# Kernel optimization log

Hardware: AMD Instinct MI355X
Metric: run time of the kernel (lower is better)

Reference implementation:

```python
import jax, jax.numpy as jnp
import numpy as np

EPS = 1e-12  # matches torch F.normalize clamp_min eps


def agnn_conv(x, src, dst, beta, num_nodes):
    # x: [N, H]; src/dst: [E'] (self-loops already included)
    norm = jnp.sqrt(jnp.sum(x * x, axis=-1, keepdims=True))
    x_norm = x / jnp.maximum(norm, EPS)
    # edge-wise cosine similarity scaled by beta
    logits = beta * jnp.sum(x_norm[src] * x_norm[dst], axis=-1)  # [E']
    # scatter-softmax over incoming edges of each destination node
    m = jax.ops.segment_max(logits, dst, num_segments=num_nodes)  # [N]
    e = jnp.exp(logits - m[dst])
    s = jax.ops.segment_sum(e, dst, num_segments=num_nodes)       # [N]
    alpha = e / s[dst]                                            # [E']
    # weighted scatter-add aggregation of source features
    return jax.ops.segment_sum(alpha[:, None] * x[src], dst, num_segments=num_nodes)


def setup_inputs() -> dict:
    key = jax.random.key(0)
    ks = jax.random.split(key, 8)
    N, E, C_in, C_hid, C_out = 100000, 1600000, 512, 128, 64
    x = jax.random.normal(ks[0], (N, C_in), dtype=jnp.float32)
    edge_index = jax.random.randint(ks[1], (2, E), 0, N, dtype=jnp.int64)
    W1 = jax.random.normal(ks[2], (C_in, C_hid), dtype=jnp.float32) / np.sqrt(C_in)
    b1 = jnp.zeros((C_hid,), dtype=jnp.float32)
    W2 = jax.random.normal(ks[3], (C_hid, C_out), dtype=jnp.float32) / np.sqrt(C_hid)
    b2 = jnp.zeros((C_out,), dtype=jnp.float32)
    beta2 = jnp.array(1.0, dtype=jnp.float32)  # learned beta of prop2; prop1 beta fixed at 1.0
    return {"x": x, "edge_index": edge_index, "W1": W1, "b1": b1,
            "beta2": beta2, "W2": W2, "b2": b2}


def reference(x, edge_index, W1, b1, beta2, W2, b2):
    N = x.shape[0]
    # AGNNConv adds self-loops by default
    loops = jnp.arange(N, dtype=edge_index.dtype)
    src = jnp.concatenate([edge_index[0], loops])
    dst = jnp.concatenate([edge_index[1], loops])
    # dropout is identity in eval mode
    h = jax.nn.relu(x @ W1 + b1)                      # [N, hidden]
    h = agnn_conv(h, src, dst, jnp.float32(1.0), N)   # prop1 (beta frozen = 1)
    h = agnn_conv(h, src, dst, beta2, N)              # prop2 (learned beta)
    logits = h @ W2 + b2                              # [N, out]
    return jax.nn.log_softmax(logits, axis=1)
```

## Files before the change

### kernel.cpp

```cpp
#include <hip/hip_runtime.h>
#include <hip/hip_fp8.h>
#include <math.h>


static inline int divup(int a, int b) { return (a + b - 1) / b; }

typedef __attribute__((ext_vector_type(8))) short short8;
typedef __attribute__((ext_vector_type(4))) float f32x4;
union U16 { uint4 u; short8 s; };

__device__ __forceinline__ unsigned bf16r(float f) {
    unsigned u = __float_as_uint(f);
    return (u + 0x7FFFu + ((u >> 16) & 1u)) >> 16;
}
__device__ __forceinline__ unsigned pack2(float a, float b) {
    return bf16r(a) | (bf16r(b) << 16);
}
__device__ __forceinline__ float bflo(unsigned u) { return __uint_as_float(u << 16); }
__device__ __forceinline__ float bfhi(unsigned u) { return __uint_as_float(u & 0xFFFF0000u); }

__device__ __forceinline__ unsigned char fp8e(float f) {
    __hip_fp8_e4m3 q(f);
    return (unsigned char)q.__x;
}
__device__ __forceinline__ float fp8d(unsigned char b) {
    __hip_fp8_e4m3 q;
    q.__x = (__hip_fp8_storage_t)b;
    return (float)q;
}
__device__ __forceinline__ void unpf8(uint2 u, float* v) {
    const unsigned char* b = (const unsigned char*)&u;
#pragma unroll
    for (int i = 0; i < 8; ++i) v[i] = fp8d(b[i]);
}

__global__ __launch_bounds__(64) void k_detect(const int* __restrict__ raw, int* flag) {
    int t = threadIdx.x;
    int v = raw[2 * t + 1];
    unsigned long long b = __ballot(v != 0);
    if (t == 0) *flag = (b == 0ULL) ? 1 : 0;
}

__global__ __launch_bounds__(256) void k_cvt(const int* __restrict__ raw, int E,
                                             const int* __restrict__ flag,
                                             int* __restrict__ s32, int* __restrict__ d32,
                                             int* __restrict__ cnt) {
    int i = blockIdx.x * blockDim.x + threadIdx.x;
    if (i >= E) return;
    int s, d;
    if (*flag) {
        s = raw[2 * (size_t)i];
        d = raw[2 * ((size_t)E + i)];
    } else {
        s = raw[i];
        d = raw[(size_t)E + i];
    }
    s32[i] = s;
    d32[i] = d;
    atomicAdd(&cnt[d], 1);
}

__global__ __launch_bounds__(1024) void k_scan1(const int* __restrict__ cnt, int N,
                                                int* __restrict__ rp, int* __restrict__ bsum) {
    __shared__ int sm[1024];
    int t = threadIdx.x;
    int i = blockIdx.x * 1024 + t;
    int v = (i < N) ? cnt[i] + 1 : 0;
    sm[t] = v;
    __syncthreads();
#pragma unroll
    for (int off = 1; off < 1024; off <<= 1) {
        int u = (t >= off) ? sm[t - off] : 0;
        __syncthreads();
        sm[t] += u;
        __syncthreads();
    }
    if (i < N) rp[i] = sm[t] - v;
    if (t == 1023) bsum[blockIdx.x] = sm[t];
}

__global__ __launch_bounds__(64) void k_scan2(int* __restrict__ bsum, int nb) {
    if (threadIdx.x == 0) {
        int run = 0;
        for (int i = 0; i < nb; ++i) { int v = bsum[i]; bsum[i] = run; run += v; }
    }
}

__global__ __launch_bounds__(256) void k_scan3(int* __restrict__ rp, const int* __restrict__ bsum,
                                               int N, int Etot, int* __restrict__ cursor) {
    int i = blockIdx.x * blockDim.x + threadIdx.x;
    if (i < N) {
        int v = rp[i] + bsum[i >> 10];
        rp[i] = v;
        cursor[i] = v;
    } else if (i == N) {
        rp[N] = Etot;
    }
}

__global__ __launch_bounds__(256) void k_scatter(const int* __restrict__ s32,
                                                 const int* __restrict__ d32, int E, int N,
                                                 int* __restrict__ cursor,
                                                 int* __restrict__ esrc) {
    int b = blockIdx.x;
    int xcd = b & 7;
    int nstripe = gridDim.x >> 3;
    int stripe = b >> 3;
    int lo = (int)(((long long)xcd * N) >> 3);
    int hi = (int)(((long long)(xcd + 1) * N) >> 3);
    int Etot = E + N;
    for (int e = stripe * 256 + threadIdx.x; e < Etot; e += nstripe * 256) {
        int d = (e < E) ? d32[e] : (e - E);
        if (d < lo || d >= hi) continue;
        int s = (e < E) ? s32[e] : d;
        int pos = atomicAdd(&cursor[d], 1);
        esrc[pos] = s;
    }
}

__global__ __launch_bounds__(256) void k_cvtW1(const float* __restrict__ W1,
                                               unsigned short* __restrict__ W1t) {
    int i = blockIdx.x * 256 + threadIdx.x;
    if (i >= 512 * 128) return;
    int k = i >> 7, n = i & 127;
    W1t[n * 512 + k] = (unsigned short)bf16r(W1[i]);
}

__global__ __launch_bounds__(256) void k_cvtW2(const float* __restrict__ W2,
                                               unsigned short* __restrict__ W2t) {
    int i = blockIdx.x * 256 + threadIdx.x;
    if (i >= 128 * 64) return;
    int k = i >> 6, n = i & 63;
    W2t[n * 128 + k] = (unsigned short)bf16r(W2[i]);
}

#define XSW(c, off) ((off) ^ (((c) & 7) << 4))
__global__ __launch_bounds__(256) void k_gemm1(const float* __restrict__ x,
                                               const unsigned short* __restrict__ W1t,
                                               const float* __restrict__ b1, int N,
                                               unsigned char* __restrict__ xh1,
                                               float* __restrict__ n1) {
    __shared__ __align__(16) unsigned char lds[32768];
    const int tid = threadIdx.x;
    const int lane = tid & 63;
    const int lt = lane & 15, lg = lane >> 4;
    const int w = tid >> 6;
    const int row0 = blockIdx.x * 64;

    int arow = row0 + w * 16 + lt;
    if (arow > N - 1) arow = N - 1;
    const float* xb = x + (size_t)arow * 512 + lg * 8;

    f32x4 acc[8];
#pragma unroll
    for (int j = 0; j < 8; ++j) acc[j] = (f32x4){0.f, 0.f, 0.f, 0.f};

    float4 buf[4][2];
#pragma unroll
    for (int j = 0; j < 4; ++j) {
        buf[j][0] = ((const float4*)(xb + j * 32))[0];
        buf[j][1] = ((const float4*)(xb + j * 32))[1];
    }

#pragma unroll 1
    for (int kt = 0; kt < 4; ++kt) {
        const int kb = kt * 128;
        __syncthreads();
        {
            int c = tid >> 1, h = tid & 1;
            const uint4* wp = (const uint4*)(W1t + c * 512 + kb + h * 64);
            unsigned char* base = lds + c * 256;
#pragma unroll
            for (int i = 0; i < 8; ++i)
                *(uint4*)(base + XSW(c, h * 128 + i * 16)) = wp[i];
        }
        __syncthreads();

        const bool more = kt < 3;
#pragma unroll
        for (int j = 0; j < 4; ++j) {
            U16 af;
            af.u.x = pack2(buf[j][0].x, buf[j][0].y);
            af.u.y = pack2(buf[j][0].z, buf[j][0].w);
            af.u.z = pack2(buf[j][1].x, buf[j][1].y);
            af.u.w = pack2(buf[j][1].z, buf[j][1].w);
            if (more) {
                const float* np = xb + (kt + 1) * 128 + j * 32;
                buf[j][0] = ((const float4*)np)[0];
                buf[j][1] = ((const float4*)np)[1];
            }
#pragma unroll
            for (int cf = 0; cf < 8; ++cf) {
                int col = cf * 16 + lt;
                U16 bf;
                bf.u = *(const uint4*)(lds + col * 256 + XSW(col, j * 64 + lg * 16));
                acc[cf] = __builtin_amdgcn_mfma_f32_16x16x32_bf16(
                    af.s, bf.s, acc[cf], 0, 0, 0);
            }
        }
    }

    float bias[8];
#pragma unroll
    for (int cf = 0; cf < 8; ++cf) bias[cf] = b1[cf * 16 + lt];
    float* sc = (float*)lds;
    unsigned char* pk = lds + 16896;
#pragma unroll 1
    for (int p = 0; p < 2; ++p) {
        __syncthreads();
        if ((w >> 1) == p) {
#pragma unroll
            for (int reg = 0; reg < 4; ++reg) {
                int rl = (w & 1) * 16 + lg * 4 + reg;
#pragma unroll
                for (int cf = 0; cf < 8; ++cf)
                    sc[rl * 132 + cf * 16 + lt] =
                        fmaxf(acc[cf][reg] + bias[cf], 0.f);
            }
        }
        __syncthreads();
        {
            int rl = tid >> 3, q = tid & 7;
            int gr = row0 + p * 32 + rl;
            const float* rowp = sc + rl * 132 + q * 16;
            float v[16];
#pragma unroll
            for (int i = 0; i < 4; ++i) {
                float4 f = ((const float4*)rowp)[i];
                v[4 * i] = f.x; v[4 * i + 1] = f.y; v[4 * i + 2] = f.z; v[4 * i + 3] = f.w;
            }
            float s2 = 0.f;
#pragma unroll
            for (int i = 0; i < 16; ++i) s2 += v[i] * v[i];
            s2 += __shfl_xor(s2, 1, 64);
            s2 += __shfl_xor(s2, 2, 64);
            s2 += __shfl_xor(s2, 4, 64);
            float nrm = sqrtf(s2);
            float rn = 1.0f / fmaxf(nrm, 1e-12f);
            union { unsigned char b[16]; uint4 u; } O;
#pragma unroll
            for (int i = 0; i < 16; ++i) O.b[i] = fp8e(v[i] * rn);
            *(uint4*)(pk + rl * 144 + q * 16) = O.u;
            if (q == 0 && gr < N) n1[gr] = nrm;
        }
        __syncthreads();
        {
            int boff = tid * 16;
            int r = boff >> 7;
            int inner = boff & 127;
            int gr = row0 + p * 32 + r;
            if (gr < N)
                *(uint4*)(xh1 + (size_t)gr * 128 + inner) =
                    *(const uint4*)(pk + r * 144 + inner);
        }
    }
}

__global__ __launch_bounds__(256) void k_conv(const unsigned char* __restrict__ xh,
                                              const float* __restrict__ nrmt,
                                              const int* __restrict__ rp,
                                              const int* __restrict__ esrc, int N,
                                              const float* __restrict__ betap,
                                              unsigned char* __restrict__ outf8,
                                              float* __restrict__ outn,
                                              unsigned short* __restrict__ outbf) {
    int node = (blockIdx.x * blockDim.x + threadIdx.x) >> 6;
    if (node >= N) return;
    int lane = threadIdx.x & 63;
    int t = lane & 15, g = lane >> 4;
    float beta = betap ? *betap : 1.0f;

    uint2 hdu = *(const uint2*)&xh[(size_t)node * 128 + 8 * t];
    float hd[8];
    unpf8(hdu, hd);

    int e0 = rp[node], e1 = rp[node + 1];
    float acc[8] = {0.f, 0.f, 0.f, 0.f, 0.f, 0.f, 0.f, 0.f};
    float ssum = 0.f;

    for (int cs = e0; cs < e1; cs += 64) {
        int el = cs + lane;
        int sidx = esrc[(el < e1) ? el : e0];
        float nsl = nrmt[sidx];
        int R = e1 - cs;
        if (R > 64) R = 64;
        int nr = (R + 3) >> 2;

        int sA = __shfl(sidx, g, 64);
        float nsA = __shfl(nsl, g, 64);
        uint2 rowA = *(const uint2*)&xh[(size_t)sA * 128 + 8 * t];

        for (int r = 0; r < nr; ++r) {
            const bool hasNext = (r + 1) < nr;
            uint2 rowB;
            float nsB = 0.f;
            if (hasNext) {
                int sB = __shfl(sidx, 4 * (r + 1) + g, 64);
                nsB = __shfl(nsl, 4 * (r + 1) + g, 64);
                rowB = *(const uint2*)&xh[(size_t)sB * 128 + 8 * t];
            }
            float v[8];
            unpf8(rowA, v);
            float p = 0.f;
#pragma unroll
            for (int j = 0; j < 8; ++j) p += v[j] * hd[j];
            p += __shfl_xor(p, 1, 64);
            p += __shfl_xor(p, 2, 64);
            p += __shfl_xor(p, 4, 64);
            p += __shfl_xor(p, 8, 64);
            int e = cs + 4 * r + g;
            float w = (e < e1) ? __expf(p * beta) : 0.f;
            float wn = w * nsA;
            ssum += w;
#pragma unroll
            for (int j = 0; j < 8; ++j) acc[j] += wn * v[j];
            if (hasNext) {
                rowA = rowB;
                nsA = nsB;
            }
        }
    }
#pragma unroll
    for (int j = 0; j < 8; ++j) {
        acc[j] += __shfl_xor(acc[j], 16, 64);
        acc[j] += __shfl_xor(acc[j], 32, 64);
    }
    ssum += __shfl_xor(ssum, 16, 64);
    ssum += __shfl_xor(ssum, 32, 64);
    float r = 1.0f / ssum;

    if (outbf != nullptr) {
        if (g == 0) {
            uint4 q;
            q.x = pack2(acc[0] * r, acc[1] * r);
            q.y = pack2(acc[2] * r, acc[3] * r);
            q.z = pack2(acc[4] * r, acc[5] * r);
            q.w = pack2(acc[6] * r, acc[7] * r);
            *(uint4*)&outbf[(size_t)node * 128 + 8 * t] = q;
        }
    } else {
        float o[8];
        float s2 = 0.f;
#pragma unroll
        for (int j = 0; j < 8; ++j) { o[j] = acc[j] * r; s2 += o[j] * o[j]; }
        s2 += __shfl_xor(s2, 1, 64);
        s2 += __shfl_xor(s2, 2, 64);
        s2 += __shfl_xor(s2, 4, 64);
        s2 += __shfl_xor(s2, 8, 64);
        float nn = sqrtf(s2);
        float rn = 1.0f / fmaxf(nn, 1e-12f);
        if (g == 0) {
            union { unsigned char b[8]; uint2 u; } O;
#pragma unroll
            for (int j = 0; j < 8; ++j) O.b[j] = fp8e(o[j] * rn);
            *(uint2*)&outf8[(size_t)node * 128 + 8 * t] = O.u;
            if (t == 0) outn[node] = nn;
        }
    }
}

#define G2_ASTRIDE 272
__global__ __launch_bounds__(256) void k_gemm2(const unsigned short* __restrict__ h,
                                               const unsigned short* __restrict__ W2t,
                                               const float* __restrict__ b2, int N,
                                               float* __restrict__ out) {
    __shared__ __align__(16) unsigned char As[128 * G2_ASTRIDE];
    __shared__ __align__(16) unsigned char Bs[64 * G2_ASTRIDE];
    const int tid = threadIdx.x;
    const int lane = tid & 63;
    const int lt = lane & 15, lg = lane >> 4;
    const int wid = tid >> 6;
    const int row0 = blockIdx.x * 128;

    {
        int arow = tid >> 1, ahalf = tid & 1;
        const uint4* src = (const uint4*)(h + (size_t)(row0 + arow) * 128 + ahalf * 64);
        unsigned char* ab = As + arow * G2_ASTRIDE + ahalf * 128;
#pragma unroll
        for (int i = 0; i < 8; ++i) ((uint4*)ab)[i] = src[i];
        int brow = tid >> 2, bq = tid & 3;
        const uint4* bs = (const uint4*)(W2t + (size_t)brow * 128 + bq * 32);
        unsigned char* bb = Bs + brow * G2_ASTRIDE + bq * 64;
#pragma unroll
        for (int i = 0; i < 4; ++i) ((uint4*)bb)[i] = bs[i];
    }
    __syncthreads();

    f32x4 acc[2][4];
#pragma unroll
    for (int i = 0; i < 2; ++i)
#pragma unroll
        for (int j = 0; j < 4; ++j) acc[i][j] = (f32x4){0.f, 0.f, 0.f, 0.f};

#pragma unroll
    for (int sub = 0; sub < 4; ++sub) {
        U16 af[2], bf[4];
#pragma unroll
        for (int mi = 0; mi < 2; ++mi)
            af[mi].u = *(const uint4*)(As + (wid * 32 + mi * 16 + lt) * G2_ASTRIDE + sub * 64 + lg * 16);
#pragma unroll
        for (int ni = 0; ni < 4; ++ni)
            bf[ni].u = *(const uint4*)(Bs + (ni * 16 + lt) * G2_ASTRIDE + sub * 64 + lg * 16);
#pragma unroll
        for (int mi = 0; mi < 2; ++mi)
#pragma unroll
            for (int ni = 0; ni < 4; ++ni)
                acc[mi][ni] = __builtin_amdgcn_mfma_f32_16x16x32_bf16(
                    af[mi].s, bf[ni].s, acc[mi][ni], 0, 0, 0);
    }

    float bias[4];
#pragma unroll
    for (int ni = 0; ni < 4; ++ni) bias[ni] = b2[ni * 16 + lt];

#pragma unroll
    for (int mi = 0; mi < 2; ++mi) {
#pragma unroll
        for (int reg = 0; reg < 4; ++reg) {
            int row = row0 + wid * 32 + mi * 16 + lg * 4 + reg;
            if (row < N) {
                float v[4];
#pragma unroll
                for (int ni = 0; ni < 4; ++ni) v[ni] = acc[mi][ni][reg] + bias[ni];
                float m = fmaxf(fmaxf(v[0], v[1]), fmaxf(v[2], v[3]));
                m = fmaxf(m, __shfl_xor(m, 1, 64));
                m = fmaxf(m, __shfl_xor(m, 2, 64));
                m = fmaxf(m, __shfl_xor(m, 4, 64));
                m = fmaxf(m, __shfl_xor(m, 8, 64));
                float s = __expf(v[0] - m) + __expf(v[1] - m) +
                          __expf(v[2] - m) + __expf(v[3] - m);
                s += __shfl_xor(s, 1, 64);
                s += __shfl_xor(s, 2, 64);
                s += __shfl_xor(s, 4, 64);
                s += __shfl_xor(s, 8, 64);
                float lg2 = logf(s);
#pragma unroll
                for (int ni = 0; ni < 4; ++ni)
                    out[(size_t)row * 64 + ni * 16 + lt] = v[ni] - m - lg2;
            }
        }
    }
}

extern "C" void kernel_launch(void* const* d_in, const int* in_sizes, int n_in,
                              void* d_out, int out_size, void* d_ws, size_t ws_size,
                              hipStream_t stream) {
    const float* x     = (const float*)d_in[0];
    const int*   ei    = (const int*)d_in[1];
    const float* W1    = (const float*)d_in[2];
    const float* b1    = (const float*)d_in[3];
    const float* beta2 = (const float*)d_in[4];
    const float* W2    = (const float*)d_in[5];
    const float* b2    = (const float*)d_in[6];
    float* out = (float*)d_out;

    const int N = in_sizes[0] / 512;
    const int E = in_sizes[1] / 2;
    const int Etot = E + N;

    char* ws = (char*)d_ws;
    size_t off = 0;
    auto alloc = [&](size_t bytes) -> void* {
        void* p = ws + off;
        off = (off + bytes + 511) & ~(size_t)511;
        return p;
    };
    unsigned char* t1  = (unsigned char*)alloc((size_t)N * 128);
    unsigned char* t2  = (unsigned char*)alloc((size_t)N * 128);
    unsigned short* h3 = (unsigned short*)alloc((size_t)N * 128 * 2);
    float* n1   = (float*)alloc((size_t)N * 4);
    float* n2   = (float*)alloc((size_t)N * 4);
    int* cnt    = (int*)alloc((size_t)N * 4);
    int* rp     = (int*)alloc((size_t)(N + 1) * 4);
    int* cursor = (int*)alloc((size_t)N * 4);
    int* bsum   = (int*)alloc(4096);
    int* flag   = (int*)alloc(512);
    unsigned short* W1t = (unsigned short*)alloc(512 * 128 * 2);
    unsigned short* W2t = (unsigned short*)alloc(128 * 64 * 2);
    int* s32    = (int*)alloc((size_t)E * 4);
    int* d32    = (int*)alloc((size_t)E * 4);
    int* esrc   = (int*)alloc((size_t)Etot * 4);
    (void)ws_size; (void)n_in; (void)out_size;

    (void)hipMemsetAsync(cnt, 0, (size_t)N * 4, stream);

    k_detect<<<1, 64, 0, stream>>>(ei, flag);
    k_cvt<<<divup(E, 256), 256, 0, stream>>>(ei, E, flag, s32, d32, cnt);
    int nb = divup(N, 1024);
    k_scan1<<<nb, 1024, 0, stream>>>(cnt, N, rp, bsum);
    k_scan2<<<1, 64, 0, stream>>>(bsum, nb);
    k_scan3<<<divup(N + 1, 256), 256, 0, stream>>>(rp, bsum, N, Etot, cursor);
    k_scatter<<<2048, 256, 0, stream>>>(s32, d32, E, N, cursor, esrc);

    k_cvtW1<<<divup(512 * 128, 256), 256, 0, stream>>>(W1, W1t);
    k_cvtW2<<<divup(128 * 64, 256), 256, 0, stream>>>(W2, W2t);

    k_gemm1<<<divup(N, 64), 256, 0, stream>>>(x, W1t, b1, N, t1, n1);
    k_conv<<<divup(N, 4), 256, 0, stream>>>(t1, n1, rp, esrc, N, nullptr, t2, n2, nullptr);
    k_conv<<<divup(N, 4), 256, 0, stream>>>(t2, n2, rp, esrc, N, beta2, nullptr, nullptr, h3);
    k_gemm2<<<divup(N, 128), 256, 0, stream>>>(h3, W2t, b2, N, out);
}
```

Before: 380.3 us.

## Process 8 edges per wave step with 16-byte row loads in conv

The conv kernel now splits each wave into 8 groups of 8 lanes, and each lane loads 16 fp8 features (uint4) per source row. Previously it used 4 groups of 16 lanes loading 8 bytes each. This halves the number of inner-loop iterations and dot-product shuffle steps per edge chunk and widens the memory accesses, at the cost of more registers per lane and one extra cross-group reduction at the end. Separately, the tiny detect kernel is folded into k_cvt, where each block recomputes the index-format flag, which removes one launch.

```diff
diff --git a/kernel.cpp b/kernel.cpp
--- a/kernel.cpp
+++ b/kernel.cpp
@@ -28,27 +28,28 @@
     q.__x = (__hip_fp8_storage_t)b;
     return (float)q;
 }
-__device__ __forceinline__ void unpf8(uint2 u, float* v) {
+__device__ __forceinline__ void unpf16(uint4 u, float* v) {
     const unsigned char* b = (const unsigned char*)&u;
 #pragma unroll
-    for (int i = 0; i < 8; ++i) v[i] = fp8d(b[i]);
-}
-
-__global__ __launch_bounds__(64) void k_detect(const int* __restrict__ raw, int* flag) {
-    int t = threadIdx.x;
-    int v = raw[2 * t + 1];
-    unsigned long long b = __ballot(v != 0);
-    if (t == 0) *flag = (b == 0ULL) ? 1 : 0;
+    for (int i = 0; i < 16; ++i) v[i] = fp8d(b[i]);
 }
 
 __global__ __launch_bounds__(256) void k_cvt(const int* __restrict__ raw, int E,
-                                             const int* __restrict__ flag,
                                              int* __restrict__ s32, int* __restrict__ d32,
                                              int* __restrict__ cnt) {
-    int i = blockIdx.x * blockDim.x + threadIdx.x;
+    __shared__ int sflag;
+    int tid = threadIdx.x;
+    if (tid < 64) {
+        int v = raw[2 * tid + 1];
+        unsigned long long b = __ballot(v != 0);
+        if (tid == 0) sflag = (b == 0ULL) ? 1 : 0;
+    }
+    __syncthreads();
+    int flag = sflag;
+    int i = blockIdx.x * blockDim.x + tid;
     if (i >= E) return;
     int s, d;
-    if (*flag) {
+    if (flag) {
         s = raw[2 * (size_t)i];
         d = raw[2 * ((size_t)E + i)];
     } else {
@@ -267,15 +268,17 @@
     int node = (blockIdx.x * blockDim.x + threadIdx.x) >> 6;
     if (node >= N) return;
     int lane = threadIdx.x & 63;
-    int t = lane & 15, g = lane >> 4;
+    int t = lane & 7, g = lane >> 3;
     float beta = betap ? *betap : 1.0f;
 
-    uint2 hdu = *(const uint2*)&xh[(size_t)node * 128 + 8 * t];
-    float hd[8];
-    unpf8(hdu, hd);
+    uint4 hdu = *(const uint4*)&xh[(size_t)node * 128 + 16 * t];
+    float hd[16];
+    unpf16(hdu, hd);
 
     int e0 = rp[node], e1 = rp[node + 1];
-    float acc[8] = {0.f, 0.f, 0.f, 0.f, 0.f, 0.f, 0.f, 0.f};
+    float acc[16];
+#pragma unroll
+    for (int j = 0; j < 16; ++j) acc[j] = 0.f;
     float ssum = 0.f;
 
     for (int cs = e0; cs < e1; cs += 64) {
@@ -284,36 +287,35 @@
         float nsl = nrmt[sidx];
         int R = e1 - cs;
         if (R > 64) R = 64;
-        int nr = (R + 3) >> 2;
+        int nr = (R + 7) >> 3;
 
         int sA = __shfl(sidx, g, 64);
         float nsA = __shfl(nsl, g, 64);
-        uint2 rowA = *(const uint2*)&xh[(size_t)sA * 128 + 8 * t];
+        uint4 rowA = *(const uint4*)&xh[(size_t)sA * 128 + 16 * t];
 
         for (int r = 0; r < nr; ++r) {
             const bool hasNext = (r + 1) < nr;
-            uint2 rowB;
+            uint4 rowB;
             float nsB = 0.f;
             if (hasNext) {
-                int sB = __shfl(sidx, 4 * (r + 1) + g, 64);
-                nsB = __shfl(nsl, 4 * (r + 1) + g, 64);
-                rowB = *(const uint2*)&xh[(size_t)sB * 128 + 8 * t];
-            }
-            float v[8];
-            unpf8(rowA, v);
+                int sB = __shfl(sidx, 8 * (r + 1) + g, 64);
+                nsB = __shfl(nsl, 8 * (r + 1) + g, 64);
+                rowB = *(const uint4*)&xh[(size_t)sB * 128 + 16 * t];
+            }
+            float v[16];
+            unpf16(rowA, v);
             float p = 0.f;
 #pragma unroll
-            for (int j = 0; j < 8; ++j) p += v[j] * hd[j];
+            for (int j = 0; j < 16; ++j) p += v[j] * hd[j];
             p += __shfl_xor(p, 1, 64);
             p += __shfl_xor(p, 2, 64);
             p += __shfl_xor(p, 4, 64);
-            p += __shfl_xor(p, 8, 64);
-            int e = cs + 4 * r + g;
+            int e = cs + 8 * r + g;
             float w = (e < e1) ? __expf(p * beta) : 0.f;
             float wn = w * nsA;
             ssum += w;
 #pragma unroll
-            for (int j = 0; j < 8; ++j) acc[j] += wn * v[j];
+            for (int j = 0; j < 16; ++j) acc[j] += wn * v[j];
             if (hasNext) {
                 rowA = rowB;
                 nsA = nsB;
@@ -321,39 +323,46 @@
         }
     }
 #pragma unroll
-    for (int j = 0; j < 8; ++j) {
+    for (int j = 0; j < 16; ++j) {
+        acc[j] += __shfl_xor(acc[j], 8, 64);
         acc[j] += __shfl_xor(acc[j], 16, 64);
         acc[j] += __shfl_xor(acc[j], 32, 64);
     }
+    ssum += __shfl_xor(ssum, 8, 64);
     ssum += __shfl_xor(ssum, 16, 64);
     ssum += __shfl_xor(ssum, 32, 64);
     float r = 1.0f / ssum;
 
     if (outbf != nullptr) {
         if (g == 0) {
-            uint4 q;
-            q.x = pack2(acc[0] * r, acc[1] * r);
-            q.y = pack2(acc[2] * r, acc[3] * r);
-            q.z = pack2(acc[4] * r, acc[5] * r);
-            q.w = pack2(acc[6] * r, acc[7] * r);
-            *(uint4*)&outbf[(size_t)node * 128 + 8 * t] = q;
+            uint4 q0, q1;
+            q0.x = pack2(acc[0] * r, acc[1] * r);
+            q0.y = pack2(acc[2] * r, acc[3] * r);
+            q0.z = pack2(acc[4] * r, acc[5] * r);
+            q0.w = pack2(acc[6] * r, acc[7] * r);
+            q1.x = pack2(acc[8] * r, acc[9] * r);
+            q1.y = pack2(acc[10] * r, acc[11] * r);
+            q1.z = pack2(acc[12] * r, acc[13] * r);
+            q1.w = pack2(acc[14] * r, acc[15] * r);
+            uint4* dst = (uint4*)&outbf[(size_t)node * 128 + 16 * t];
+            dst[0] = q0;
+            dst[1] = q1;
         }
     } else {
-        float o[8];
+        float o[16];
         float s2 = 0.f;
 #pragma unroll
-        for (int j = 0; j < 8; ++j) { o[j] = acc[j] * r; s2 += o[j] * o[j]; }
+        for (int j = 0; j < 16; ++j) { o[j] = acc[j] * r; s2 += o[j] * o[j]; }
         s2 += __shfl_xor(s2, 1, 64);
         s2 += __shfl_xor(s2, 2, 64);
         s2 += __shfl_xor(s2, 4, 64);
-        s2 += __shfl_xor(s2, 8, 64);
         float nn = sqrtf(s2);
         float rn = 1.0f / fmaxf(nn, 1e-12f);
         if (g == 0) {
-            union { unsigned char b[8]; uint2 u; } O;
-#pragma unroll
-            for (int j = 0; j < 8; ++j) O.b[j] = fp8e(o[j] * rn);
-            *(uint2*)&outf8[(size_t)node * 128 + 8 * t] = O.u;
+            union { unsigned char b[16]; uint4 u; } O;
+#pragma unroll
+            for (int j = 0; j < 16; ++j) O.b[j] = fp8e(o[j] * rn);
+            *(uint4*)&outf8[(size_t)node * 128 + 16 * t] = O.u;
             if (t == 0) outn[node] = nn;
         }
     }
@@ -474,7 +483,6 @@
     int* rp     = (int*)alloc((size_t)(N + 1) * 4);
     int* cursor = (int*)alloc((size_t)N * 4);
     int* bsum   = (int*)alloc(4096);
-    int* flag   = (int*)alloc(512);
     unsigned short* W1t = (unsigned short*)alloc(512 * 128 * 2);
     unsigned short* W2t = (unsigned short*)alloc(128 * 64 * 2);
     int* s32    = (int*)alloc((size_t)E * 4);
@@ -484,8 +492,7 @@
 
     (void)hipMemsetAsync(cnt, 0, (size_t)N * 4, stream);
 
-    k_detect<<<1, 64, 0, stream>>>(ei, flag);
-    k_cvt<<<divup(E, 256), 256, 0, stream>>>(ei, E, flag, s32, d32, cnt);
+    k_cvt<<<divup(E, 256), 256, 0, stream>>>(ei, E, s32, d32, cnt);
     int nb = divup(N, 1024);
     k_scan1<<<nb, 1024, 0, stream>>>(cnt, N, rp, bsum);
     k_scan2<<<1, 64, 0, stream>>>(bsum, nb);
```

New measurement: 426.7 us. 12.2% more time.
